# Performance work log

Hardware: AMD Instinct MI355X
Metric: run time of the kernel (lower is better)

Reference implementation:

```python
import jax, jax.numpy as jnp
import numpy as np

NT, NF, CIN, COUT = 1_500_000, 500_000, 32, 32
BN_EPS = 1e-5


def setup_inputs() -> dict:
    key = jax.random.key(0)
    k1, k2, k3 = jax.random.split(key, 3)
    input_texture = jax.random.normal(k1, (NT, CIN), dtype=jnp.float32)
    # barycentric coefficients: nonnegative, rows sum to 1
    b = jax.random.uniform(k2, (NT, 3), dtype=jnp.float32) + 1e-3
    bary_coeff = b / b.sum(axis=1, keepdims=True)
    # 3 texture samples per facet (sum == NT)
    num_texture = jnp.full((NF,), 3, dtype=jnp.int32)
    # xavier-normal init for [Cout, Cin, 3] kernel
    fan = CIN * 3 + COUT * 3
    std = float(np.sqrt(2.0 / fan))
    weights = jax.random.normal(k3, (COUT, CIN, 3), dtype=jnp.float32) * std
    bias = jnp.zeros((1, COUT), dtype=jnp.float32)
    gamma = jnp.ones((COUT,), dtype=jnp.float32)
    beta = jnp.zeros((COUT,), dtype=jnp.float32)
    return {"input_texture": input_texture, "bary_coeff": bary_coeff,
            "num_texture": num_texture, "weights": weights, "bias": bias,
            "gamma": gamma, "beta": beta}


def reference(input_texture, bary_coeff, num_texture, weights, bias, gamma, beta):
    nf = num_texture.shape[0]
    nt = input_texture.shape[0]
    # segment id for each ragged texture sample (original op uses cumsum offsets)
    seg = jnp.repeat(jnp.arange(nf), num_texture, total_repeat_length=nt)
    # per-sample contribution: y[t,o] = sum_{c,k} x[t,c] * b[t,k] * W[o,c,k]
    y = jnp.einsum('tc,tk,ock->to', input_texture, bary_coeff, weights)
    # facet2facet averages over the samples of each facet
    s = jax.ops.segment_sum(y, seg, num_segments=nf)  # [Nf, Cout]
    cnt = jnp.maximum(num_texture.astype(y.dtype), 1)[:, None]
    out = s / cnt
    out = out + bias          # bias add
    out = jax.nn.relu(out)    # activation
    # BatchNorm1d in training mode: batch statistics over the facet dim
    mean = out.mean(axis=0)
    var = out.var(axis=0)
    out = (out - mean) * jax.lax.rsqrt(var + BN_EPS) * gamma + beta
    return out
```

## Files before the change

kernel.cpp:

```cpp
#include <hip/hip_runtime.h>
#include <hip/hip_bf16.h>
#include <stdint.h>

typedef __attribute__((ext_vector_type(4))) float fv4;
typedef float fv4u __attribute__((ext_vector_type(4), aligned(4)));
typedef __attribute__((ext_vector_type(4))) short sv4;
typedef __attribute__((ext_vector_type(8))) short sv8;

typedef __attribute__((address_space(3))) float lds_f;
typedef __attribute__((address_space(1))) const float glb_f;

#define SCHUNK 2048
#define NIT 4
#define SPAN (4 * NIT * 16)

static __device__ __forceinline__ short f2bf(float f) {
  __hip_bfloat16 h = __float2bfloat16(f);
  union { __hip_bfloat16 h; short s; } u; u.h = h;
  return u.s;
}

__global__ __launch_bounds__(256) void scan1(const int* __restrict__ num, int nf,
                                             int* __restrict__ bsum) {
  __shared__ int sd[256];
  int b = blockIdx.x, tid = threadIdx.x;
  int base = b * SCHUNK + tid * 8;
  int s = 0;
#pragma unroll
  for (int j = 0; j < 8; ++j) { int i = base + j; if (i < nf) s += num[i]; }
  sd[tid] = s; __syncthreads();
  for (int st = 128; st > 0; st >>= 1) {
    if (tid < st) sd[tid] += sd[tid + st];
    __syncthreads();
  }
  if (tid == 0) bsum[b] = sd[0];
}

__global__ __launch_bounds__(256) void scan2(int* __restrict__ bsum, int nb) {
  __shared__ int sd[256];
  int tid = threadIdx.x;
  int v = (tid < nb) ? bsum[tid] : 0;
  sd[tid] = v; __syncthreads();
  for (int off = 1; off < 256; off <<= 1) {
    int t = (tid >= off) ? sd[tid - off] : 0;
    __syncthreads();
    sd[tid] += t;
    __syncthreads();
  }
  if (tid < nb) bsum[tid] = sd[tid] - v;
}

__global__ __launch_bounds__(256) void scan3(const int* __restrict__ num, int nf,
                                             const int* __restrict__ bsum,
                                             int* __restrict__ offsets) {
  __shared__ int sc_[256];
  int b = blockIdx.x, tid = threadIdx.x;
  int base = b * SCHUNK + tid * 8;
  int loc[8]; int s = 0;
#pragma unroll
  for (int j = 0; j < 8; ++j) {
    loc[j] = (base + j < nf) ? num[base + j] : 0;
    s += loc[j];
  }
  sc_[tid] = s; __syncthreads();
  for (int off = 1; off < 256; off <<= 1) {
    int t = (tid >= off) ? sc_[tid - off] : 0;
    __syncthreads();
    sc_[tid] += t;
    __syncthreads();
  }
  int run = bsum[b] + sc_[tid] - s;
#pragma unroll
  for (int j = 0; j < 8; ++j) {
    if (base + j < nf) offsets[base + j] = run;
    run += loc[j];
  }
  if (b == gridDim.x - 1 && tid == 255) offsets[nf] = run;
}

__global__ __launch_bounds__(256) void k_prep(const float* __restrict__ W,
                                              short* __restrict__ w2g) {
  for (int i = threadIdx.x; i < 3072; i += 256) {
    int o = i / 96;
    int ck = i - o * 96;
    int k = ck >> 5, c = ck & 31;
    w2g[o * 96 + ck] = f2bf(W[o * 96 + c * 3 + k]);
  }
}

#define DECL_RS(S) \
  int st_##S, en_##S; \
  float bb0_##S, bb1_##S, bb2_##S, bb3_##S, bb4_##S, bb5_##S, bb6_##S, bb7_##S, bb8_##S;

#define LOADR(S, T) do { \
  const int f_ = blk0w + (T) * 16 + rowl; \
  const int fa_ = f_ < nf ? f_ : nf; \
  const int fb_ = (f_ + 1) < nf ? (f_ + 1) : nf; \
  st_##S = offsets[fa_]; \
  en_##S = offsets[fb_]; \
  const int s3_ = 3 * f_; \
  const int sb_ = (f_ < nf && s3_ + 3 <= nt) ? s3_ : 0; \
  const float* bp_ = bary + (size_t)sb_ * 3; \
  fv4u bv0_ = *(const fv4u*)(bp_); \
  fv4u bv1_ = *(const fv4u*)(bp_ + 4); \
  bb0_##S = bv0_[0]; bb1_##S = bv0_[1]; bb2_##S = bv0_[2]; \
  bb3_##S = bv0_[3]; bb4_##S = bv1_[0]; bb5_##S = bv1_[1]; \
  bb6_##S = bv1_[2]; bb7_##S = bv1_[3]; bb8_##S = bp_[8]; \
} while (0)

#define STAGE(T, BUFSEL) do { \
  const int f0t_ = blk0w + (T) * 16; \
  long r0_ = 3L * f0t_; \
  long br_ = (r0_ + 48 <= nt) ? r0_ : (nt >= 48 ? (long)nt - 48 : 0); \
  const float* gx_ = x + br_ * 32; \
  float* lb_ = Xw0 + (BUFSEL) * 1536; \
  _Pragma("unroll") \
  for (int i_ = 0; i_ < 6; ++i_) { \
    int L_ = i_ * 64 + lane; \
    int G_ = L_ ^ ((L_ >> 3) & 7); \
    __builtin_amdgcn_global_load_lds((glb_f*)(gx_ + G_ * 4), (lds_f*)(lb_ + i_ * 256), 16, 0, 0); \
  } \
} while (0)

#define WAITV do { \
  asm volatile("s_waitcnt vmcnt(0)" ::: "memory"); \
  __builtin_amdgcn_sched_barrier(0); \
} while (0)

#define COMPUTE(S, T, BUFSEL) do { \
  const int f0t = blk0w + (T) * 16; \
  const int f_ = f0t + rowl; \
  const int nm_my = en_##S - st_##S; \
  const bool dense_ = (3L * f0t + 48 <= nt); \
  float z0[8], z1[8], z2[8]; \
  _Pragma("unroll") \
  for (int j = 0; j < 8; ++j) { z0[j] = 0.f; z1[j] = 0.f; z2[j] = 0.f; } \
  if (dense_ && nm_my == 3 && st_##S == 3 * f_) { \
    const float* Xb_ = Xw0 + (BUFSEL) * 1536; \
    _Pragma("unroll") \
    for (int s_ = 0; s_ < 3; ++s_) { \
      int row_ = 3 * rowl + s_; \
      int sw_ = row_ & 7; \
      fv4 xa = *(const fv4*)(Xb_ + (((row_ * 8 + grp) ^ sw_) << 2)); \
      fv4 xb = *(const fv4*)(Xb_ + (((row_ * 8 + 4 + grp) ^ sw_) << 2)); \
      float b0_ = (s_ == 0) ? bb0_##S : (s_ == 1) ? bb3_##S : bb6_##S; \
      float b1_ = (s_ == 0) ? bb1_##S : (s_ == 1) ? bb4_##S : bb7_##S; \
      float b2_ = (s_ == 0) ? bb2_##S : (s_ == 1) ? bb5_##S : bb8_##S; \
      _Pragma("unroll") \
      for (int j = 0; j < 4; ++j) { \
        z0[j]     += xa[j] * b0_; z1[j]     += xa[j] * b1_; z2[j]     += xa[j] * b2_; \
        z0[4 + j] += xb[j] * b0_; z1[4 + j] += xb[j] * b1_; z2[4 + j] += xb[j] * b2_; \
      } \
    } \
  } else { \
    for (int t2 = st_##S; t2 < en_##S; ++t2) { \
      const float* xp = x + (size_t)t2 * 32; \
      fv4 xa = *(const fv4*)(xp + cb_lo); \
      fv4 xb = *(const fv4*)(xp + cb_hi); \
      const float* bpp = bary + (size_t)t2 * 3; \
      float b0_ = bpp[0], b1_ = bpp[1], b2_ = bpp[2]; \
      _Pragma("unroll") \
      for (int j = 0; j < 4; ++j) { \
        z0[j]     += xa[j] * b0_; z1[j]     += xa[j] * b1_; z2[j]     += xa[j] * b2_; \
        z0[4 + j] += xb[j] * b0_; z1[4 + j] += xb[j] * b1_; z2[4 + j] += xb[j] * b2_; \
      } \
    } \
  } \
  fv4 acc0 = (fv4){0.f, 0.f, 0.f, 0.f}; \
  fv4 acc1 = (fv4){0.f, 0.f, 0.f, 0.f}; \
  _Pragma("unroll") \
  for (int kb = 0; kb < 3; ++kb) { \
    sv8 afr; \
    _Pragma("unroll") \
    for (int j = 0; j < 4; ++j) { \
      float lo = (kb == 0) ? z0[j]     : (kb == 1) ? z1[j]     : z2[j]; \
      float hi = (kb == 0) ? z0[4 + j] : (kb == 1) ? z1[4 + j] : z2[4 + j]; \
      afr[j]     = f2bf(lo); \
      afr[4 + j] = f2bf(hi); \
    } \
    acc0 = __builtin_amdgcn_mfma_f32_16x16x32_bf16(afr, bfrA[kb], acc0, 0, 0, 0); \
    acc1 = __builtin_amdgcn_mfma_f32_16x16x32_bf16(afr, bfrB[kb], acc1, 0, 0, 0); \
  } \
  _Pragma("unroll") \
  for (int r = 0; r < 4; ++r) { \
    int row = grp * 4 + r; \
    int fr = f0t + row; \
    int nm = __shfl(nm_my, row, 64); \
    float inv = 1.0f / (float)(nm > 1 ? nm : 1); \
    if (fr < nf) { \
      float v0 = fmaxf(acc0[r] * inv + bo0, 0.f); \
      float v1 = fmaxf(acc1[r] * inv + bo1, 0.f); \
      out[fr * 32 + rowl]      = v0; \
      out[fr * 32 + 16 + rowl] = v1; \
      s1l += v0; s2l += v0 * v0; \
      s1h += v1; s2h += v1 * v1; \
    } \
  } \
} while (0)

__global__ __launch_bounds__(256, 3) void k_main(
    const float* __restrict__ x, const float* __restrict__ bary,
    const short* __restrict__ w2g, const float* __restrict__ bias,
    const int* __restrict__ offsets, float* __restrict__ out,
    float* __restrict__ partials, int nf, int nt, int nw)
{
  __shared__ __align__(16) float Xs[4 * 2 * 1536];

  const int tid = threadIdx.x;
  const int lane = tid & 63;
  const int wv = tid >> 6;
  float* Xw0 = &Xs[wv * 3072];

  const int rowl = lane & 15;
  const int grp = lane >> 4;
  const int cb_lo = grp * 4;
  const int cb_hi = grp * 4 + 16;
  const int blk0w = blockIdx.x * SPAN + wv * (NIT * 16);

  sv8 bfrA[3], bfrB[3];
#pragma unroll
  for (int kb = 0; kb < 3; ++kb) {
    const int cko = kb * 32 + grp * 4;
    {
      const short* wr = w2g + rowl * 96 + cko;
      sv4 lo = *(const sv4*)(wr), hi = *(const sv4*)(wr + 16);
#pragma unroll
      for (int j = 0; j < 4; ++j) { bfrA[kb][j] = lo[j]; bfrA[kb][4 + j] = hi[j]; }
    }
    {
      const short* wr = w2g + (16 + rowl) * 96 + cko;
      sv4 lo = *(const sv4*)(wr), hi = *(const sv4*)(wr + 16);
#pragma unroll
      for (int j = 0; j < 4; ++j) { bfrB[kb][j] = lo[j]; bfrB[kb][4 + j] = hi[j]; }
    }
  }

  float bo0 = bias[rowl];
  float bo1 = bias[16 + rowl];
  float s1l = 0.f, s1h = 0.f, s2l = 0.f, s2h = 0.f;

  const bool can_stage = (nt >= 48);

  DECL_RS(A)
  DECL_RS(B)

  if (can_stage) STAGE(0, 0);
  LOADR(A, 0);

  WAITV;
  if (can_stage) STAGE(1, 1);
  LOADR(B, 1);
  COMPUTE(A, 0, 0);
  WAITV;
  if (can_stage) STAGE(2, 0);
  LOADR(A, 2);
  COMPUTE(B, 1, 1);
  WAITV;
  if (can_stage) STAGE(3, 1);
  LOADR(B, 3);
  COMPUTE(A, 2, 0);
  WAITV;
  COMPUTE(B, 3, 1);

  s1l += __shfl_xor(s1l, 16, 64); s1l += __shfl_xor(s1l, 32, 64);
  s1h += __shfl_xor(s1h, 16, 64); s1h += __shfl_xor(s1h, 32, 64);
  s2l += __shfl_xor(s2l, 16, 64); s2l += __shfl_xor(s2l, 32, 64);
  s2h += __shfl_xor(s2h, 16, 64); s2h += __shfl_xor(s2h, 32, 64);
  if (grp == 0) {
    int w = blockIdx.x * 4 + wv;
    partials[(long)(rowl)      * nw + w] = s1l;
    partials[(long)(16 + rowl) * nw + w] = s1h;
    partials[(long)(32 + rowl) * nw + w] = s2l;
    partials[(long)(48 + rowl) * nw + w] = s2h;
  }
}

__global__ __launch_bounds__(256) void k_reduce(const float* __restrict__ partials,
                                                int nw, float* __restrict__ stats) {
  __shared__ float sd[256];
  int c = blockIdx.x;
  const float* p = partials + (long)c * nw;
  float s = 0.f;
  for (int i = threadIdx.x; i < nw; i += 256) s += p[i];
  sd[threadIdx.x] = s; __syncthreads();
  for (int st = 128; st > 0; st >>= 1) {
    if (threadIdx.x < st) sd[threadIdx.x] += sd[threadIdx.x + st];
    __syncthreads();
  }
  if (threadIdx.x == 0) stats[c] = sd[0];
}

__global__ __launch_bounds__(256) void k_bn(float* __restrict__ out,
                                            const float* __restrict__ stats,
                                            const float* __restrict__ gamma,
                                            const float* __restrict__ beta, int nf) {
  __shared__ float sc[32], sh[32];
  if (threadIdx.x < 32) {
    int o = threadIdx.x;
    float inv_n = 1.0f / (float)nf;
    float mean = stats[o] * inv_n;
    float var = stats[32 + o] * inv_n - mean * mean;
    float rstd = rsqrtf(var + 1e-5f);
    float g = gamma[o] * rstd;
    sc[o] = g;
    sh[o] = beta[o] - mean * g;
  }
  __syncthreads();
  long total4 = (long)nf * 8;
  long idx0 = (long)blockIdx.x * 256 + threadIdx.x;
  int ob = ((int)idx0 & 7) * 4;
  fv4 scv = *(const fv4*)&sc[ob];
  fv4 shv = *(const fv4*)&sh[ob];
  for (long idx = idx0; idx < total4; idx += (long)gridDim.x * 256) {
    fv4 v = *((const fv4*)out + idx);
    v = v * scv + shv;
    *((fv4*)out + idx) = v;
  }
}

extern "C" void kernel_launch(void* const* d_in, const int* in_sizes, int n_in,
                              void* d_out, int out_size, void* d_ws, size_t ws_size,
                              hipStream_t stream) {
  const float* x     = (const float*)d_in[0];
  const float* bary  = (const float*)d_in[1];
  const int*   numt  = (const int*)d_in[2];
  const float* W     = (const float*)d_in[3];
  const float* bias  = (const float*)d_in[4];
  const float* gamma = (const float*)d_in[5];
  const float* beta  = (const float*)d_in[6];
  float* out = (float*)d_out;

  const int nf   = in_sizes[2];
  const int nt   = in_sizes[0] / 32;
  const int nblk = (nf + SPAN - 1) / SPAN;
  const int nw   = nblk * 4;
  const int nbS  = (nf + SCHUNK - 1) / SCHUNK;

  char* w = (char*)d_ws;
  int* offsets = (int*)w;
  size_t off1 = (4UL * (size_t)(nf + 1) + 255) & ~255UL;
  int* bsum = (int*)(w + off1);
  size_t off2 = (off1 + 4UL * (size_t)nbS + 255) & ~255UL;
  short* w2g = (short*)(w + off2);
  size_t off3 = (off2 + 2UL * 3072UL + 255) & ~255UL;
  float* partials = (float*)(w + off3);
  size_t off4 = (off3 + 4UL * 64UL * (size_t)nw + 255) & ~255UL;
  float* stats = (float*)(w + off4);

  scan1<<<nbS, 256, 0, stream>>>(numt, nf, bsum);
  scan2<<<1, 256, 0, stream>>>(bsum, nbS);
  scan3<<<nbS, 256, 0, stream>>>(numt, nf, bsum, offsets);
  k_prep<<<1, 256, 0, stream>>>(W, w2g);
  k_main<<<nblk, 256, 0, stream>>>(x, bary, w2g, bias, offsets, out, partials, nf, nt, nw);
  k_reduce<<<64, 256, 0, stream>>>(partials, nw, stats);
  k_bn<<<2048, 256, 0, stream>>>(out, stats, gamma, beta, nf);
}
```

Baseline: 101.4 us.

## Deepen async staging pipeline, stage bary via LDS, coalesce output stores

Each wave now handles twice as many 16-facet tiles, and the loop keeps two tiles in flight using partial vmcnt waits instead of draining all loads before each compute. Barycentric coefficients are copied into LDS asynchronously alongside the texture rows rather than loaded per lane. Output tiles are written through an LDS transpose buffer so each wave issues contiguous 16-byte stores. The extra LDS use lowers the occupancy hint from 3 to 2 blocks per CU, and the hand-counted vmcnt values must match the real number of outstanding loads or the kernel will read stale data.

```diff
diff --git a/kernel.cpp b/kernel.cpp
--- a/kernel.cpp
+++ b/kernel.cpp
@@ -3,7 +3,6 @@
 #include <stdint.h>
 
 typedef __attribute__((ext_vector_type(4))) float fv4;
-typedef float fv4u __attribute__((ext_vector_type(4), aligned(4)));
 typedef __attribute__((ext_vector_type(4))) short sv4;
 typedef __attribute__((ext_vector_type(8))) short sv8;
 
@@ -11,7 +10,7 @@
 typedef __attribute__((address_space(1))) const float glb_f;
 
 #define SCHUNK 2048
-#define NIT 4
+#define NIT 8
 #define SPAN (4 * NIT * 16)
 
 static __device__ __forceinline__ short f2bf(float f) {
@@ -88,9 +87,30 @@
   }
 }
 
-#define DECL_RS(S) \
-  int st_##S, en_##S; \
-  float bb0_##S, bb1_##S, bb2_##S, bb3_##S, bb4_##S, bb5_##S, bb6_##S, bb7_##S, bb8_##S;
+#define WAITN_(N) do { \
+  asm volatile("s_waitcnt vmcnt(" #N ")" ::: "memory"); \
+  __builtin_amdgcn_sched_barrier(0); \
+} while (0)
+#define WAITN(N) WAITN_(N)
+
+#define STAGE(T, BUF) do { \
+  if (can_stage) { \
+    const int f0t_ = blk0w + (T) * 16; \
+    long r0_ = 3L * f0t_; \
+    long br_ = (r0_ + 48 <= (long)nt) ? r0_ : (long)nt - 48; \
+    const float* gx_ = x + br_ * 32; \
+    float* lb_ = &Xs[wv][BUF][0]; \
+    _Pragma("unroll") \
+    for (int i_ = 0; i_ < 6; ++i_) { \
+      int L_ = i_ * 64 + lane; \
+      int G_ = L_ ^ ((L_ >> 3) & 7); \
+      __builtin_amdgcn_global_load_lds((glb_f*)(gx_ + G_ * 4), (lds_f*)(lb_ + i_ * 256), 16, 0, 0); \
+    } \
+    const float* gb_ = bary + br_ * 3; \
+    if (lane < 36) \
+      __builtin_amdgcn_global_load_lds((glb_f*)(gb_ + lane * 4), (lds_f*)(&Bs[wv][BUF][0]), 16, 0, 0); \
+  } \
+} while (0)
 
 #define LOADR(S, T) do { \
   const int f_ = blk0w + (T) * 16 + rowl; \
@@ -98,54 +118,30 @@
   const int fb_ = (f_ + 1) < nf ? (f_ + 1) : nf; \
   st_##S = offsets[fa_]; \
   en_##S = offsets[fb_]; \
-  const int s3_ = 3 * f_; \
-  const int sb_ = (f_ < nf && s3_ + 3 <= nt) ? s3_ : 0; \
-  const float* bp_ = bary + (size_t)sb_ * 3; \
-  fv4u bv0_ = *(const fv4u*)(bp_); \
-  fv4u bv1_ = *(const fv4u*)(bp_ + 4); \
-  bb0_##S = bv0_[0]; bb1_##S = bv0_[1]; bb2_##S = bv0_[2]; \
-  bb3_##S = bv0_[3]; bb4_##S = bv1_[0]; bb5_##S = bv1_[1]; \
-  bb6_##S = bv1_[2]; bb7_##S = bv1_[3]; bb8_##S = bp_[8]; \
 } while (0)
 
-#define STAGE(T, BUFSEL) do { \
-  const int f0t_ = blk0w + (T) * 16; \
-  long r0_ = 3L * f0t_; \
-  long br_ = (r0_ + 48 <= nt) ? r0_ : (nt >= 48 ? (long)nt - 48 : 0); \
-  const float* gx_ = x + br_ * 32; \
-  float* lb_ = Xw0 + (BUFSEL) * 1536; \
-  _Pragma("unroll") \
-  for (int i_ = 0; i_ < 6; ++i_) { \
-    int L_ = i_ * 64 + lane; \
-    int G_ = L_ ^ ((L_ >> 3) & 7); \
-    __builtin_amdgcn_global_load_lds((glb_f*)(gx_ + G_ * 4), (lds_f*)(lb_ + i_ * 256), 16, 0, 0); \
-  } \
-} while (0)
-
-#define WAITV do { \
-  asm volatile("s_waitcnt vmcnt(0)" ::: "memory"); \
-  __builtin_amdgcn_sched_barrier(0); \
-} while (0)
-
-#define COMPUTE(S, T, BUFSEL) do { \
+#define PART(S, T, BUF, STG, WN) do { \
+  WAITN(WN); \
   const int f0t = blk0w + (T) * 16; \
   const int f_ = f0t + rowl; \
   const int nm_my = en_##S - st_##S; \
-  const bool dense_ = (3L * f0t + 48 <= nt); \
+  const bool dense_ = can_stage && (3L * f0t + 48 <= (long)nt); \
+  const bool dense_st = (f0t + 16 <= nf); \
   float z0[8], z1[8], z2[8]; \
   _Pragma("unroll") \
   for (int j = 0; j < 8; ++j) { z0[j] = 0.f; z1[j] = 0.f; z2[j] = 0.f; } \
   if (dense_ && nm_my == 3 && st_##S == 3 * f_) { \
-    const float* Xb_ = Xw0 + (BUFSEL) * 1536; \
+    const float* Xb_ = &Xs[wv][BUF][0]; \
+    const float* bb_ = &Bs[wv][BUF][9 * rowl]; \
     _Pragma("unroll") \
     for (int s_ = 0; s_ < 3; ++s_) { \
       int row_ = 3 * rowl + s_; \
       int sw_ = row_ & 7; \
       fv4 xa = *(const fv4*)(Xb_ + (((row_ * 8 + grp) ^ sw_) << 2)); \
       fv4 xb = *(const fv4*)(Xb_ + (((row_ * 8 + 4 + grp) ^ sw_) << 2)); \
-      float b0_ = (s_ == 0) ? bb0_##S : (s_ == 1) ? bb3_##S : bb6_##S; \
-      float b1_ = (s_ == 0) ? bb1_##S : (s_ == 1) ? bb4_##S : bb7_##S; \
-      float b2_ = (s_ == 0) ? bb2_##S : (s_ == 1) ? bb5_##S : bb8_##S; \
+      float b0_ = bb_[3 * s_ + 0]; \
+      float b1_ = bb_[3 * s_ + 1]; \
+      float b2_ = bb_[3 * s_ + 2]; \
       _Pragma("unroll") \
       for (int j = 0; j < 4; ++j) { \
         z0[j]     += xa[j] * b0_; z1[j]     += xa[j] * b1_; z2[j]     += xa[j] * b2_; \
@@ -181,35 +177,57 @@
     acc0 = __builtin_amdgcn_mfma_f32_16x16x32_bf16(afr, bfrA[kb], acc0, 0, 0, 0); \
     acc1 = __builtin_amdgcn_mfma_f32_16x16x32_bf16(afr, bfrB[kb], acc1, 0, 0, 0); \
   } \
+  float* yw = &Yt[wv][0]; \
   _Pragma("unroll") \
   for (int r = 0; r < 4; ++r) { \
     int row = grp * 4 + r; \
     int fr = f0t + row; \
     int nm = __shfl(nm_my, row, 64); \
     float inv = 1.0f / (float)(nm > 1 ? nm : 1); \
-    if (fr < nf) { \
-      float v0 = fmaxf(acc0[r] * inv + bo0, 0.f); \
-      float v1 = fmaxf(acc1[r] * inv + bo1, 0.f); \
+    float v0 = fmaxf(acc0[r] * inv + bo0, 0.f); \
+    float v1 = fmaxf(acc1[r] * inv + bo1, 0.f); \
+    if (dense_st) { \
+      yw[row * 32 + rowl]      = v0; \
+      yw[row * 32 + 16 + rowl] = v1; \
+      s1l += v0; s2l += v0 * v0; \
+      s1h += v1; s2h += v1 * v1; \
+    } else if (fr < nf) { \
       out[fr * 32 + rowl]      = v0; \
       out[fr * 32 + 16 + rowl] = v1; \
       s1l += v0; s2l += v0 * v0; \
       s1h += v1; s2h += v1 * v1; \
     } \
   } \
+  if (dense_st) { \
+    __builtin_amdgcn_wave_barrier(); \
+    const float* yr = &Yt[wv][0]; \
+    fv4 o0 = *(const fv4*)(yr + lane * 4); \
+    fv4 o1 = *(const fv4*)(yr + 256 + lane * 4); \
+    float* op = out + (size_t)f0t * 32; \
+    *(fv4*)(op + lane * 4)       = o0; \
+    *(fv4*)(op + 256 + lane * 4) = o1; \
+    __builtin_amdgcn_wave_barrier(); \
+  } \
+  if (STG) { \
+    __builtin_amdgcn_sched_barrier(0); \
+    STAGE((T) + 2, BUF); \
+    LOADR(S, (T) + 2); \
+  } \
 } while (0)
 
-__global__ __launch_bounds__(256, 3) void k_main(
+__global__ __launch_bounds__(256, 2) void k_main(
     const float* __restrict__ x, const float* __restrict__ bary,
     const short* __restrict__ w2g, const float* __restrict__ bias,
     const int* __restrict__ offsets, float* __restrict__ out,
     float* __restrict__ partials, int nf, int nt, int nw)
 {
-  __shared__ __align__(16) float Xs[4 * 2 * 1536];
+  __shared__ __align__(16) float Xs[4][2][1536];
+  __shared__ __align__(16) float Bs[4][2][256];
+  __shared__ __align__(16) float Yt[4][512];
 
   const int tid = threadIdx.x;
   const int lane = tid & 63;
   const int wv = tid >> 6;
-  float* Xw0 = &Xs[wv * 3072];
 
   const int rowl = lane & 15;
   const int grp = lane >> 4;
@@ -241,26 +259,19 @@
 
   const bool can_stage = (nt >= 48);
 
-  DECL_RS(A)
-  DECL_RS(B)
-
-  if (can_stage) STAGE(0, 0);
+  int st_A, en_A, st_B, en_B;
+
+  STAGE(0, 0);
   LOADR(A, 0);
-
-  WAITV;
-  if (can_stage) STAGE(1, 1);
+  STAGE(1, 1);
   LOADR(B, 1);
-  COMPUTE(A, 0, 0);
-  WAITV;
-  if (can_stage) STAGE(2, 0);
-  LOADR(A, 2);
-  COMPUTE(B, 1, 1);
-  WAITV;
-  if (can_stage) STAGE(3, 1);
-  LOADR(B, 3);
-  COMPUTE(A, 2, 0);
-  WAITV;
-  COMPUTE(B, 3, 1);
+
+  for (int t = 0; t < NIT - 2; t += 2) {
+    PART(A, t, 0, 1, 11);
+    PART(B, t + 1, 1, 1, 11);
+  }
+  PART(A, NIT - 2, 0, 0, 11);
+  PART(B, NIT - 1, 1, 0, 2);
 
   s1l += __shfl_xor(s1l, 16, 64); s1l += __shfl_xor(s1l, 32, 64);
   s1h += __shfl_xor(s1h, 16, 64); s1h += __shfl_xor(s1h, 32, 64);
```

Measured after the change: 96.22 us. -5.1%, faster.
